# Kernel optimization log

Measured on AMD Instinct MI355X. Metric: run time of the kernel, lower is better.

Reference implementation:

```python
import jax, jax.numpy as jnp
import numpy as np

N = 100000
E = 500000
LATENT = 256
EDGE_DIM = 128
HIDDEN = 2 * EDGE_DIM  # 256


def setup_inputs() -> dict:
    key = jax.random.key(0)
    k_z, k_e, k_w1, k_b1, k_w2, k_b2 = jax.random.split(key, 6)
    z = jax.random.normal(k_z, (N, LATENT), dtype=jnp.float32)
    edge_index = jax.random.randint(k_e, (2, E), 0, N, dtype=jnp.int64)
    # torch nn.Linear init: U(-1/sqrt(fan_in), 1/sqrt(fan_in))
    lim1 = 1.0 / np.sqrt(2 * LATENT)
    W1 = jax.random.uniform(k_w1, (HIDDEN, 2 * LATENT), jnp.float32, -lim1, lim1)
    b1 = jax.random.uniform(k_b1, (HIDDEN,), jnp.float32, -lim1, lim1)
    lim2 = 1.0 / np.sqrt(HIDDEN)
    W2 = jax.random.uniform(k_w2, (EDGE_DIM, HIDDEN), jnp.float32, -lim2, lim2)
    b2 = jax.random.uniform(k_b2, (EDGE_DIM,), jnp.float32, -lim2, lim2)
    return {"z": z, "edge_index": edge_index, "W1": W1, "b1": b1, "W2": W2, "b2": b2}


def reference(z, edge_index, W1, b1, W2, b2):
    # Gather endpoint embeddings and concat: [E, 2*latent]
    src = z[edge_index[0]]
    dst = z[edge_index[1]]
    pair = jnp.concatenate([src, dst], axis=1)
    # 2-layer MLP (dropout is identity in eval mode)
    h = jax.nn.relu(pair @ W1.T + b1)
    out = h @ W2.T + b2  # [E, edge_dim]
    return out
```

## Files before the change

kernel.cpp:

```cpp
#include <hip/hip_runtime.h>
#include <hip/hip_bf16.h>

#define N_NODES 100000
#define N_EDGES 500000

typedef __attribute__((ext_vector_type(8))) short  short8;
typedef __attribute__((ext_vector_type(4))) short  short4v;
typedef __attribute__((ext_vector_type(4))) float  float4v;

__device__ __forceinline__ unsigned short f2bf(float f) {
    union { float f; unsigned int u; } v; v.f = f;
    unsigned int u = v.u;
    unsigned int r = u + 0x7fffu + ((u >> 16) & 1u);
    return (unsigned short)(r >> 16);
}
__device__ __forceinline__ float bf2f(unsigned short b) {
    union { unsigned int u; float f; } v; v.u = ((unsigned int)b) << 16;
    return v.f;
}

__device__ __forceinline__ void gload_lds16(const unsigned short* g, unsigned short* l) {
    __builtin_amdgcn_global_load_lds(
        (const __attribute__((address_space(1))) unsigned int*)g,
        (__attribute__((address_space(3))) unsigned int*)l, 16, 0, 0);
}

__global__ void zconv_kernel(const float* __restrict__ z, unsigned short* __restrict__ zb) {
    size_t i = ((size_t)blockIdx.x * 256 + threadIdx.x) * 8;
    float4v a = *(const float4v*)(z + i);
    float4v b = *(const float4v*)(z + i + 4);
    short8 o;
    o[0] = (short)f2bf(a.x); o[1] = (short)f2bf(a.y); o[2] = (short)f2bf(a.z); o[3] = (short)f2bf(a.w);
    o[4] = (short)f2bf(b.x); o[5] = (short)f2bf(b.y); o[6] = (short)f2bf(b.z); o[7] = (short)f2bf(b.w);
    *(short8*)(zb + i) = o;
}

__global__ void prep_kernel(const float* __restrict__ W1, const float* __restrict__ W2,
                            unsigned short* __restrict__ w1c, unsigned short* __restrict__ w2b) {
    int j = blockIdx.x, k = threadIdx.x;
    if (j < 512) {
        float v = (j < 256) ? W1[(size_t)j * 512 + k] : W1[(size_t)(j - 256) * 512 + 256 + k];
        w1c[(size_t)j * 256 + k] = f2bf(v);
    } else {
        int o = j - 512;
        w2b[(size_t)o * 256 + k] = f2bf(W2[(size_t)o * 256 + k]);
    }
}

__launch_bounds__(256, 2)
__global__ void stage1_kernel(const unsigned short* __restrict__ zb,
                              const unsigned short* __restrict__ w1c,
                              unsigned short* __restrict__ ZW) {
    __shared__ unsigned short lds[128 * 136];
    unsigned short* At = lds;
    unsigned short* Bt = lds + 128 * 64;

    const int t    = threadIdx.x;
    const int lane = t & 63, wave = t >> 6;
    const int wm = wave >> 1, wn = wave & 1;
    const int l15 = lane & 15, quad = lane >> 4;
    const int mbase = blockIdx.x * 128, nbase = blockIdx.y * 128;

    const int lr = lane >> 3;
    const int cg = (lane & 7) ^ lr;
    const unsigned short* ag[4]; const unsigned short* bg[4];
    unsigned short* al[4]; unsigned short* bl[4];
#pragma unroll
    for (int q = 0; q < 4; ++q) {
        int rA = wave * 32 + q * 8 + lr;
        int gA = mbase + rA; if (gA >= N_NODES) gA = N_NODES - 1;
        ag[q] = zb  + (size_t)gA * 256 + cg * 8;
        bg[q] = w1c + (size_t)(nbase + rA) * 256 + cg * 8;
        al[q] = At + (wave * 4 + q) * 512 + lane * 8;
        bl[q] = Bt + (wave * 4 + q) * 512 + lane * 8;
    }

    float4v acc[4][4];
    const float4v fz = {0.f, 0.f, 0.f, 0.f};
#pragma unroll
    for (int i = 0; i < 4; ++i)
#pragma unroll
        for (int j = 0; j < 4; ++j) acc[i][j] = fz;

    for (int kk = 0; kk < 256; kk += 64) {
        __syncthreads();
#pragma unroll
        for (int q = 0; q < 4; ++q) gload_lds16(ag[q] + kk, al[q]);
#pragma unroll
        for (int q = 0; q < 4; ++q) gload_lds16(bg[q] + kk, bl[q]);
        __syncthreads();

#pragma unroll
        for (int s = 0; s < 2; ++s) {
            const int ch = ((s * 4 + quad) ^ (l15 & 7)) * 8;
            short8 af[4], bfr[4];
#pragma unroll
            for (int i = 0; i < 4; ++i)
                af[i] = *(const short8*)(At + (wm * 64 + i * 16 + l15) * 64 + ch);
#pragma unroll
            for (int j = 0; j < 4; ++j)
                bfr[j] = *(const short8*)(Bt + (wn * 64 + j * 16 + l15) * 64 + ch);
#pragma unroll
            for (int i = 0; i < 4; ++i)
#pragma unroll
                for (int j = 0; j < 4; ++j)
                    acc[i][j] = __builtin_amdgcn_mfma_f32_16x16x32_bf16(af[i], bfr[j], acc[i][j], 0, 0, 0);
        }
    }

    __syncthreads();
#pragma unroll
    for (int i = 0; i < 4; ++i)
#pragma unroll
        for (int j = 0; j < 4; ++j) {
            int row = wm * 64 + i * 16 + quad * 4;
            int col = wn * 64 + j * 16 + l15;
#pragma unroll
            for (int r = 0; r < 4; ++r)
                lds[(row + r) * 136 + col] = f2bf(acc[i][j][r]);
        }
    __syncthreads();
    for (int c = t; c < 128 * 16; c += 256) {
        int row = c >> 4, ch2 = c & 15;
        int grow = mbase + row;
        if (grow < N_NODES)
            *(short8*)(ZW + (size_t)grow * 512 + nbase + ch2 * 8) =
                *(const short8*)(lds + row * 136 + ch2 * 8);
    }
}

#define H_PITCH 264
#define EBLK 64
__launch_bounds__(256, 4)
__global__ void stage2_kernel(const int* __restrict__ eidx, const unsigned short* __restrict__ ZW,
                              const float* __restrict__ b1, const unsigned short* __restrict__ w2b,
                              const float* __restrict__ b2, float* __restrict__ out) {
    __shared__ unsigned short h[EBLK * H_PITCH];
    __shared__ int idx[128];
    const int t    = threadIdx.x;
    const int lane = t & 63, wave = t >> 6;
    const int l15 = lane & 15, quad = lane >> 4;
    const int wm = wave >> 1, wn = wave & 1;
    const int eb = blockIdx.x * EBLK;

    if (t < 128) {
        int e = eb + (t & 63); if (e >= N_EDGES) e = N_EDGES - 1;
        idx[t] = eidx[(t >> 6) * N_EDGES + e];
    }

    const unsigned short* wr[4];
#pragma unroll
    for (int j = 0; j < 4; ++j)
        wr[j] = w2b + (size_t)(wn * 64 + j * 16 + l15) * 256 + quad * 8;
    short8 bfrag[4][2];
#pragma unroll
    for (int kk = 0; kk < 2; ++kk)
#pragma unroll
        for (int j = 0; j < 4; ++j)
            bfrag[j][kk] = *(const short8*)(wr[j] + kk * 32);

    __syncthreads();

    const int lj = t & 31, er = t >> 5;
    float4v b1a = *(const float4v*)(b1 + lj * 8);
    float4v b1b = *(const float4v*)(b1 + lj * 8 + 4);
    const unsigned short* zs = ZW + lj * 8;
    const unsigned short* zd = ZW + 256 + lj * 8;

    short8 va[4], vb[4];
#pragma unroll
    for (int p = 0; p < 4; ++p) {
        int el = p * 8 + er;
        va[p] = *(const short8*)(zs + (size_t)idx[el] * 512);
        vb[p] = *(const short8*)(zd + (size_t)idx[64 + el] * 512);
    }
#pragma unroll
    for (int p = 0; p < 8; ++p) {
        int el = p * 8 + er;
        short8 xa = va[p & 3], xb = vb[p & 3];
        if (p < 4) {
            int el4 = el + 32;
            va[p & 3] = *(const short8*)(zs + (size_t)idx[el4] * 512);
            vb[p & 3] = *(const short8*)(zd + (size_t)idx[64 + el4] * 512);
        }
        short8 rv;
#pragma unroll
        for (int i = 0; i < 8; ++i) {
            float v = bf2f((unsigned short)xa[i]) + bf2f((unsigned short)xb[i])
                    + ((i < 4) ? b1a[i] : b1b[i - 4]);
            v = v > 0.f ? v : 0.f;
            rv[i] = (short)f2bf(v);
        }
        *(short8*)(h + el * H_PITCH + lj * 8) = rv;
    }
    __syncthreads();

    float4v acc[2][4];
    const float4v fz = {0.f, 0.f, 0.f, 0.f};
#pragma unroll
    for (int i = 0; i < 2; ++i)
#pragma unroll
        for (int j = 0; j < 4; ++j) acc[i][j] = fz;

    short8 pre[4];
#pragma unroll
    for (int j = 0; j < 4; ++j) pre[j] = *(const short8*)(wr[j] + 2 * 32);

#pragma unroll
    for (int kk = 0; kk < 8; ++kk) {
        short8 af[2];
#pragma unroll
        for (int i = 0; i < 2; ++i)
            af[i] = *(const short8*)(h + (wm * 32 + i * 16 + l15) * H_PITCH + kk * 32 + quad * 8);
        short8 bcur[4];
        if (kk < 2) {
#pragma unroll
            for (int j = 0; j < 4; ++j) bcur[j] = bfrag[j][kk];
        } else {
#pragma unroll
            for (int j = 0; j < 4; ++j) bcur[j] = pre[j];
            if (kk < 7) {
#pragma unroll
                for (int j = 0; j < 4; ++j) pre[j] = *(const short8*)(wr[j] + (kk + 1) * 32);
            }
        }
#pragma unroll
        for (int i = 0; i < 2; ++i)
#pragma unroll
            for (int j = 0; j < 4; ++j)
                acc[i][j] = __builtin_amdgcn_mfma_f32_16x16x32_bf16(af[i], bcur[j], acc[i][j], 0, 0, 0);
    }

#pragma unroll
    for (int j = 0; j < 4; ++j) {
        int col = wn * 64 + j * 16 + l15;
        float bias = b2[col];
#pragma unroll
        for (int i = 0; i < 2; ++i) {
            int row0 = wm * 32 + i * 16 + quad * 4;
#pragma unroll
            for (int r = 0; r < 4; ++r) {
                int e = eb + row0 + r;
                if (e < N_EDGES) out[(size_t)e * 128 + col] = acc[i][j][r] + bias;
            }
        }
    }
}

__global__ void fallback_kernel(const float* __restrict__ z, const int* __restrict__ eidx,
                                const float* __restrict__ W1, const float* __restrict__ b1,
                                const float* __restrict__ W2, const float* __restrict__ b2,
                                float* __restrict__ out) {
    __shared__ float zs[512];
    __shared__ float hh[256];
    int e = blockIdx.x, t = threadIdx.x;
    int s = eidx[e], d = eidx[N_EDGES + e];
    zs[t]       = z[(size_t)s * 256 + t];
    zs[256 + t] = z[(size_t)d * 256 + t];
    __syncthreads();
    float a = b1[t];
    const float* wr = W1 + (size_t)t * 512;
    for (int k = 0; k < 512; ++k) a += zs[k] * wr[k];
    hh[t] = a > 0.f ? a : 0.f;
    __syncthreads();
    if (t < 128) {
        float o = b2[t];
        const float* w2r = W2 + (size_t)t * 256;
        for (int k = 0; k < 256; ++k) o += hh[k] * w2r[k];
        out[(size_t)e * 128 + t] = o;
    }
}

extern "C" void kernel_launch(void* const* d_in, const int* in_sizes, int n_in,
                              void* d_out, int out_size, void* d_ws, size_t ws_size,
                              hipStream_t stream) {
    const float* z    = (const float*)d_in[0];
    const int*   eidx = (const int*)d_in[1];
    const float* W1   = (const float*)d_in[2];
    const float* b1   = (const float*)d_in[3];
    const float* W2   = (const float*)d_in[4];
    const float* b2   = (const float*)d_in[5];
    float* out = (float*)d_out;

    const size_t zw_bytes = (size_t)N_NODES * 512 * 2;
    const size_t w1c_off  = zw_bytes;
    const size_t w2b_off  = w1c_off + (size_t)512 * 256 * 2;
    const size_t need     = w2b_off + (size_t)128 * 256 * 2;

    if (ws_size < need) {
        fallback_kernel<<<N_EDGES, 256, 0, stream>>>(z, eidx, W1, b1, W2, b2, out);
        return;
    }
    unsigned short* ZW  = (unsigned short*)d_ws;
    unsigned short* w1c = (unsigned short*)((char*)d_ws + w1c_off);
    unsigned short* w2b = (unsigned short*)((char*)d_ws + w2b_off);
    unsigned short* zb  = (unsigned short*)d_out;

    zconv_kernel<<<12500, 256, 0, stream>>>(z, zb);
    prep_kernel<<<640, 256, 0, stream>>>(W1, W2, w1c, w2b);
    stage1_kernel<<<dim3(782, 4), 256, 0, stream>>>(zb, w1c, ZW);
    stage2_kernel<<<(N_EDGES + EBLK - 1) / EBLK, 256, 0, stream>>>(eidx, ZW, b1, w2b, b2, out);
}
```

Baseline: 547.3 us.

## Stage output through LDS for coalesced nontemporal stores and deepen gather prefetch

Epilogue writes MLP results into the reused LDS tile, then emits coalesced float4 nontemporal global stores per row instead of scattered scalar stores. All eight endpoint gather loads are issued upfront for more memory-level parallelism. W2 fragment loading is moved after the gather and restructured into a two-deep prefetch ring. Adds two barriers and extra registers, which may reduce occupancy.

Result: faster. 486.7 us (-11.1%).

```diff
diff --git a/kernel.cpp b/kernel.cpp
--- a/kernel.cpp
+++ b/kernel.cpp
@@ -137,6 +137,7 @@
                               const float* __restrict__ b2, float* __restrict__ out) {
     __shared__ unsigned short h[EBLK * H_PITCH];
     __shared__ int idx[128];
+    float* hf = (float*)h;
     const int t    = threadIdx.x;
     const int lane = t & 63, wave = t >> 6;
     const int l15 = lane & 15, quad = lane >> 4;
@@ -147,18 +148,6 @@
         int e = eb + (t & 63); if (e >= N_EDGES) e = N_EDGES - 1;
         idx[t] = eidx[(t >> 6) * N_EDGES + e];
     }
-
-    const unsigned short* wr[4];
-#pragma unroll
-    for (int j = 0; j < 4; ++j)
-        wr[j] = w2b + (size_t)(wn * 64 + j * 16 + l15) * 256 + quad * 8;
-    short8 bfrag[4][2];
-#pragma unroll
-    for (int kk = 0; kk < 2; ++kk)
-#pragma unroll
-        for (int j = 0; j < 4; ++j)
-            bfrag[j][kk] = *(const short8*)(wr[j] + kk * 32);
-
     __syncthreads();
 
     const int lj = t & 31, er = t >> 5;
@@ -167,9 +156,9 @@
     const unsigned short* zs = ZW + lj * 8;
     const unsigned short* zd = ZW + 256 + lj * 8;
 
-    short8 va[4], vb[4];
-#pragma unroll
-    for (int p = 0; p < 4; ++p) {
+    short8 va[8], vb[8];
+#pragma unroll
+    for (int p = 0; p < 8; ++p) {
         int el = p * 8 + er;
         va[p] = *(const short8*)(zs + (size_t)idx[el] * 512);
         vb[p] = *(const short8*)(zd + (size_t)idx[64 + el] * 512);
@@ -177,12 +166,7 @@
 #pragma unroll
     for (int p = 0; p < 8; ++p) {
         int el = p * 8 + er;
-        short8 xa = va[p & 3], xb = vb[p & 3];
-        if (p < 4) {
-            int el4 = el + 32;
-            va[p & 3] = *(const short8*)(zs + (size_t)idx[el4] * 512);
-            vb[p & 3] = *(const short8*)(zd + (size_t)idx[64 + el4] * 512);
-        }
+        short8 xa = va[p], xb = vb[p];
         short8 rv;
 #pragma unroll
         for (int i = 0; i < 8; ++i) {
@@ -195,6 +179,11 @@
     }
     __syncthreads();
 
+    const unsigned short* wr[4];
+#pragma unroll
+    for (int j = 0; j < 4; ++j)
+        wr[j] = w2b + (size_t)(wn * 64 + j * 16 + l15) * 256 + quad * 8;
+
     float4v acc[2][4];
     const float4v fz = {0.f, 0.f, 0.f, 0.f};
 #pragma unroll
@@ -202,9 +191,11 @@
 #pragma unroll
         for (int j = 0; j < 4; ++j) acc[i][j] = fz;
 
-    short8 pre[4];
-#pragma unroll
-    for (int j = 0; j < 4; ++j) pre[j] = *(const short8*)(wr[j] + 2 * 32);
+    short8 pre[4][2];
+#pragma unroll
+    for (int kk = 0; kk < 2; ++kk)
+#pragma unroll
+        for (int j = 0; j < 4; ++j) pre[j][kk] = *(const short8*)(wr[j] + kk * 32);
 
 #pragma unroll
     for (int kk = 0; kk < 8; ++kk) {
@@ -213,16 +204,11 @@
         for (int i = 0; i < 2; ++i)
             af[i] = *(const short8*)(h + (wm * 32 + i * 16 + l15) * H_PITCH + kk * 32 + quad * 8);
         short8 bcur[4];
-        if (kk < 2) {
-#pragma unroll
-            for (int j = 0; j < 4; ++j) bcur[j] = bfrag[j][kk];
-        } else {
-#pragma unroll
-            for (int j = 0; j < 4; ++j) bcur[j] = pre[j];
-            if (kk < 7) {
-#pragma unroll
-                for (int j = 0; j < 4; ++j) pre[j] = *(const short8*)(wr[j] + (kk + 1) * 32);
-            }
+#pragma unroll
+        for (int j = 0; j < 4; ++j) bcur[j] = pre[j][kk & 1];
+        if (kk < 6) {
+#pragma unroll
+            for (int j = 0; j < 4; ++j) pre[j][kk & 1] = *(const short8*)(wr[j] + (kk + 2) * 32);
         }
 #pragma unroll
         for (int i = 0; i < 2; ++i)
@@ -231,6 +217,7 @@
                 acc[i][j] = __builtin_amdgcn_mfma_f32_16x16x32_bf16(af[i], bcur[j], acc[i][j], 0, 0, 0);
     }
 
+    __syncthreads();
 #pragma unroll
     for (int j = 0; j < 4; ++j) {
         int col = wn * 64 + j * 16 + l15;
@@ -239,10 +226,19 @@
         for (int i = 0; i < 2; ++i) {
             int row0 = wm * 32 + i * 16 + quad * 4;
 #pragma unroll
-            for (int r = 0; r < 4; ++r) {
-                int e = eb + row0 + r;
-                if (e < N_EDGES) out[(size_t)e * 128 + col] = acc[i][j][r] + bias;
-            }
+            for (int r = 0; r < 4; ++r)
+                hf[(row0 + r) * 132 + col] = acc[i][j][r] + bias;
+        }
+    }
+    __syncthreads();
+#pragma unroll
+    for (int pass = 0; pass < 8; ++pass) {
+        int it  = pass * 256 + t;
+        int row = it >> 5, c4 = (it & 31) * 4;
+        int e = eb + row;
+        if (e < N_EDGES) {
+            float4v v = *(const float4v*)(hf + row * 132 + c4);
+            __builtin_nontemporal_store(v, (float4v*)(out + (size_t)e * 128 + c4));
         }
     }
 }
```
